# Kernel tuning notes

Measured on AMD Instinct MI355X. Metric: run time of the kernel, lower is better.

The kernel has to match this reference:

```python
import jax, jax.numpy as jnp
import numpy as np

N_CELLS = 50000
HID = 64
DEG = 16
K_NODES = 4  # nodes per cell; cell i owns nodes [4i, 4i+4)
SP = 3


def setup_inputs() -> dict:
    key = jax.random.key(0)
    ks = jax.random.split(key, 12)
    s = 1.0 / np.sqrt(HID)
    inp = {
        'features': jax.random.normal(ks[0], (N_CELLS, HID), jnp.float32),
        'positions': jax.random.normal(ks[1], (K_NODES * N_CELLS, SP), jnp.float32),
        'neighbors': jax.random.randint(ks[2], (N_CELLS, DEG), 0, N_CELLS, jnp.int32),
        # message MLP: Linear(2H+1 -> H), SiLU, Linear(H -> H)
        'W1': jax.random.normal(ks[3], (2 * HID + 1, HID), jnp.float32) * s,
        'b1': jnp.zeros((HID,), jnp.float32),
        'W2': jax.random.normal(ks[4], (HID, HID), jnp.float32) * s,
        'b2': jnp.zeros((HID,), jnp.float32),
        # update MLP: Linear(H + H -> H), SiLU, Linear(H -> H)
        'Wu1': jax.random.normal(ks[5], (2 * HID, HID), jnp.float32) * s,
        'bu1': jnp.zeros((HID,), jnp.float32),
        'Wu2': jax.random.normal(ks[6], (HID, HID), jnp.float32) * s,
        'bu2': jnp.zeros((HID,), jnp.float32),
    }
    return inp


def reference(features, positions, neighbors, W1, b1, W2, b2, Wu1, bu1, Wu2, bu2):
    N, H = features.shape
    # centroid of each cell's owned nodes (cell i -> nodes [K*i, K*i+K))
    cent = positions.reshape(N, K_NODES, SP).mean(axis=1)          # [N, sp]
    fj = features[neighbors]                                       # [N, D, H]
    cj = cent[neighbors]                                           # [N, D, sp]
    # centroid-distance geometric invariant per (cell, neighbor) pair
    geom = jnp.linalg.norm(cent[:, None, :] - cj, axis=-1, keepdims=True)  # [N, D, 1]
    fi = jnp.broadcast_to(features[:, None, :], fj.shape)          # [N, D, H]
    x = jnp.concatenate([fi, fj, geom], axis=-1)                   # [N, D, 2H+1]
    h = jax.nn.silu(x @ W1 + b1) @ W2 + b2                         # [N, D, H]
    msg = h.mean(axis=1)                                           # mean over neighbors
    u = jnp.concatenate([features, msg], axis=-1)                  # [N, 2H]
    upd = jax.nn.silu(u @ Wu1 + bu1) @ Wu2 + bu2
    updated_features = features + upd
    return updated_features, positions
```

## Files before the change

### kernel.cpp

```cpp
#include <hip/hip_runtime.h>


#define DEG 16

typedef __attribute__((ext_vector_type(8))) short short8;
typedef __attribute__((ext_vector_type(4))) float f32x4;
typedef uint2 uint2_a __attribute__((may_alias));
typedef uint4 uint4_a __attribute__((may_alias));

union HbRd { uint4_a u; short8 s; };
union Frag { short8 s; uint4 u; };

__device__ __forceinline__ unsigned f2bf(float f) {
  unsigned u = __float_as_uint(f);
  return (u + 0x7FFFu + ((u >> 16) & 1u)) >> 16;
}
__device__ __forceinline__ float bf2f(unsigned bits16) {
  return __uint_as_float(bits16 << 16);
}
__device__ __forceinline__ float silu(float h) {
  return h / (1.f + __expf(-h));
}
__device__ __forceinline__ float silu_fast(float h) {
  return h * __builtin_amdgcn_rcpf(1.f + __expf(-h));
}

__global__ __launch_bounds__(256) void aux_kernel(
    const float* __restrict__ pos,
    const float* __restrict__ W1, const float* __restrict__ W2,
    const float* __restrict__ Wu1, const float* __restrict__ Wu2,
    float* __restrict__ outpos, float* __restrict__ cent4,
    unsigned short* __restrict__ w1pq, unsigned short* __restrict__ w2t,
    unsigned short* __restrict__ wu1t, unsigned short* __restrict__ wu2b)
{
  int t = blockIdx.x * 256 + threadIdx.x;
  if (t < 150000) {
    ((float4*)outpos)[t] = ((const float4*)pos)[t];
  } else if (t < 174576) {
    const int r = t - 150000;
    if (r < 8192) {
      const int j = r & 7, l = (r >> 3) & 15, q = (r >> 7) & 3;
      const int f = r >> 9, kk = f & 1, mt = f >> 1;
      const int k = kk * 32 + q * 8 + j;
      const int m = mt * 16 + l;
      w1pq[r] = (unsigned short)f2bf(
          (m < 64) ? W1[k * 64 + m] : W1[(k + 64) * 64 + (m - 64)]);
    } else if (r < 12288) {
      const int s = r - 8192;
      const int j = s & 7, l = (s >> 3) & 15, q = (s >> 7) & 3;
      const int f = s >> 9, kk = f & 1, mt = f >> 1;
      const int k = kk * 32 + q * 8 + j;
      w2t[s] = (unsigned short)f2bf(W2[k * 64 + mt * 16 + l]);
    } else if (r < 20480) {
      const int s = r - 12288;
      const int j = s & 7, l = (s >> 3) & 15, q = (s >> 7) & 3;
      const int f = s >> 9, kk = f & 3, mt = f >> 2;
      const int k = kk * 32 + q * 8 + j;
      wu1t[s] = (unsigned short)f2bf(Wu1[k * 64 + mt * 16 + l]);
    } else {
      const int s = r - 20480;
      const int j = s & 7, l = (s >> 3) & 15, q = (s >> 7) & 3;
      const int f = s >> 9, kk = f & 1, nt = f >> 1;
      const int k = kk * 32 + q * 8 + j;
      wu2b[s] = (unsigned short)f2bf(Wu2[k * 64 + nt * 16 + l]);
    }
  } else if (t < 224576) {
    const int i = t - 174576;
    const float4* pp = (const float4*)(pos + 12 * i);
    const float4 a = pp[0], b = pp[1], c = pp[2];
    float4 o;
    o.x = (a.x + a.w + b.z + c.y) * 0.25f;
    o.y = (a.y + b.x + b.w + c.z) * 0.25f;
    o.z = (a.z + b.y + c.x + c.w) * 0.25f;
    o.w = 0.f;
    ((float4*)cent4)[i] = o;
  }
}

__global__ __launch_bounds__(256) void prep_geom_kernel(
    const float* __restrict__ feat,
    const unsigned short* __restrict__ w1pq,
    const float4* __restrict__ cent4,
    const int* __restrict__ nbr,
    unsigned short* __restrict__ featb,
    unsigned short* __restrict__ Pb, unsigned char* __restrict__ Q8,
    float* __restrict__ geomF)
{
  const int b    = blockIdx.x;
  const int lane = threadIdx.x & 63;
  const int wid  = threadIdx.x >> 6;

  if (b >= 782) {
    const int gb  = b - 782;
    const int sub = lane >> 4;
    const int d   = lane & 15;
    const int c   = gb * 16 + wid * 4 + sub;
    const int nj  = nbr[c * DEG + d];
    const float4 ci = cent4[c];
    const float4 cj = cent4[nj];
    const float dx = ci.x - cj.x, dy = ci.y - cj.y, dz = ci.z - cj.z;
    geomF[c * DEG + d] = sqrtf(dx * dx + dy * dy + dz * dz);
    return;
  }

  const int quad = lane >> 4;
  const int l15  = lane & 15;
  const int tile = b * 4 + wid;
  const bool act = (tile < 3125);
  const int  tt  = act ? tile : 3124;
  const int  cr  = tt * 16 + l15;

  short8 xf[2];
  #pragma unroll
  for (int kk = 0; kk < 2; ++kk) {
    const float4 f0 = *(const float4*)(feat + cr * 64 + kk * 32 + quad * 8);
    const float4 f1 = *(const float4*)(feat + cr * 64 + kk * 32 + quad * 8 + 4);
    Frag v;
    v.s[0] = (short)f2bf(f0.x); v.s[1] = (short)f2bf(f0.y);
    v.s[2] = (short)f2bf(f0.z); v.s[3] = (short)f2bf(f0.w);
    v.s[4] = (short)f2bf(f1.x); v.s[5] = (short)f2bf(f1.y);
    v.s[6] = (short)f2bf(f1.z); v.s[7] = (short)f2bf(f1.w);
    xf[kk] = v.s;
    if (act) *(uint4*)(featb + cr * 64 + kk * 32 + quad * 8) = v.u;
  }

  short8 wf[8][2];
  #pragma unroll
  for (int mt = 0; mt < 8; ++mt)
    #pragma unroll
    for (int kk = 0; kk < 2; ++kk)
      wf[mt][kk] = *(const short8*)(w1pq + (((mt * 2 + kk) * 4 + quad) << 7) + l15 * 8);

  f32x4 acc[8] = {};
  #pragma unroll
  for (int kk = 0; kk < 2; ++kk)
    #pragma unroll
    for (int mt = 0; mt < 8; ++mt)
      acc[mt] = __builtin_amdgcn_mfma_f32_16x16x32_bf16(wf[mt][kk], xf[kk], acc[mt], 0, 0, 0);

  if (act) {
    #pragma unroll
    for (int mt = 0; mt < 4; ++mt) {
      uint2 pk;
      pk.x = f2bf(acc[mt][0]) | (f2bf(acc[mt][1]) << 16);
      pk.y = f2bf(acc[mt][2]) | (f2bf(acc[mt][3]) << 16);
      *(uint2*)(Pb + cr * 64 + mt * 16 + quad * 4) = pk;
    }
    #pragma unroll
    for (int mt = 4; mt < 8; ++mt) {
      int w = __builtin_amdgcn_cvt_pk_fp8_f32(acc[mt][0], acc[mt][1], 0, false);
      w = __builtin_amdgcn_cvt_pk_fp8_f32(acc[mt][2], acc[mt][3], w, true);
      *(unsigned int*)(Q8 + cr * 64 + (mt - 4) * 16 + quad * 4) = (unsigned)w;
    }
  }
}

__global__ __launch_bounds__(256) void msg_tail_kernel(
    const unsigned short* __restrict__ featb,
    const unsigned short* __restrict__ Pb,
    const unsigned char* __restrict__ Q8,
    const float* __restrict__ geomF,
    const int* __restrict__ nbr,
    const float* __restrict__ feat,
    const unsigned short* __restrict__ w2t,
    const unsigned short* __restrict__ wu1t,
    const unsigned short* __restrict__ wu2b,
    const float* __restrict__ b1, const float* __restrict__ W1,
    const float* __restrict__ b2, const float* __restrict__ bu1,
    const float* __restrict__ bu2,
    float* __restrict__ outf)
{
  __shared__ uint4 smem[432];
  char* sT  = (char*)smem;
  char* Msg = sT + 2304;
  char* Hb  = sT + 4608;

  const int lane = threadIdx.x & 63;
  const int wid  = threadIdx.x >> 6;
  const int quad = lane >> 4;
  const int l15  = lane & 15;
  const int tile = blockIdx.x;

  const float b1l = b1[lane];
  const float wl  = W1[8192 + lane];

  #pragma unroll
  for (int i = 0; i < 4; ++i) {
    const int c  = tile * 16 + wid * 4 + i;
    const int cs = __builtin_amdgcn_readfirstlane(c);
    const int*   nrow = nbr   + cs * DEG;
    const float* grow = geomF + cs * DEG;

    const float pcb = bf2f(Pb[cs * 64 + lane]) + b1l;

    float acc = 0.f;
    #pragma unroll
    for (int d = 0; d < DEG; ++d) {
      const int   nd = nrow[d];
      const float gd = grow[d];
      const float qv = __builtin_amdgcn_cvt_f32_fp8((int)Q8[nd * 64 + lane], 0);
      acc += silu_fast(pcb + qv + gd * wl);
    }
    ((unsigned short*)(sT + (wid * 4 + i) * 144))[lane] =
        (unsigned short)f2bf(acc * 0.0625f);
  }

  short8 w2f[2], wu1f[4], wu2f[2];
  #pragma unroll
  for (int kk = 0; kk < 2; ++kk)
    w2f[kk]  = *(const short8*)(w2t  + (((wid * 2 + kk) * 4 + quad) << 7) + l15 * 8);
  #pragma unroll
  for (int kk = 0; kk < 4; ++kk)
    wu1f[kk] = *(const short8*)(wu1t + (((wid * 4 + kk) * 4 + quad) << 7) + l15 * 8);
  #pragma unroll
  for (int kk = 0; kk < 2; ++kk)
    wu2f[kk] = *(const short8*)(wu2b + (((wid * 2 + kk) * 4 + quad) << 7) + l15 * 8);

  const f32x4 b2f  = *(const f32x4*)(b2  + wid * 16 + quad * 4);
  const f32x4 bu1f = *(const f32x4*)(bu1 + wid * 16 + quad * 4);
  const float bu2v = bu2[wid * 16 + l15];

  __syncthreads();

  f32x4 accm = {};
  #pragma unroll
  for (int kk = 0; kk < 2; ++kk) {
    HbRd t; t.u = *(const uint4_a*)(sT + l15 * 144 + kk * 64 + quad * 16);
    accm = __builtin_amdgcn_mfma_f32_16x16x32_bf16(w2f[kk], t.s, accm, 0, 0, 0);
  }
  __syncthreads();
  {
    uint2 pk;
    pk.x = f2bf(accm[0] + b2f[0]) | (f2bf(accm[1] + b2f[1]) << 16);
    pk.y = f2bf(accm[2] + b2f[2]) | (f2bf(accm[3] + b2f[3]) << 16);
    *(uint2_a*)(Msg + l15 * 144 + wid * 32 + quad * 8) = pk;
  }
  __syncthreads();

  const int cr = tile * 16 + l15;
  f32x4 accu = {};
  #pragma unroll
  for (int kk = 0; kk < 4; ++kk) {
    short8 bf;
    if (kk < 2) {
      bf = *(const short8*)(featb + cr * 64 + kk * 32 + quad * 8);
    } else {
      HbRd t; t.u = *(const uint4_a*)(Msg + l15 * 144 + (kk - 2) * 64 + quad * 16);
      bf = t.s;
    }
    accu = __builtin_amdgcn_mfma_f32_16x16x32_bf16(wu1f[kk], bf, accu, 0, 0, 0);
  }
  {
    float sv[4];
    #pragma unroll
    for (int rg = 0; rg < 4; ++rg)
      sv[rg] = silu(accu[rg] + bu1f[rg]);
    uint2 pk;
    pk.x = f2bf(sv[0]) | (f2bf(sv[1]) << 16);
    pk.y = f2bf(sv[2]) | (f2bf(sv[3]) << 16);
    *(uint2_a*)(Hb + l15 * 144 + wid * 32 + quad * 8) = pk;
  }
  __syncthreads();

  f32x4 acc2 = {};
  #pragma unroll
  for (int kk = 0; kk < 2; ++kk) {
    HbRd t; t.u = *(const uint4_a*)(Hb + l15 * 144 + kk * 64 + quad * 16);
    acc2 = __builtin_amdgcn_mfma_f32_16x16x32_bf16(t.s, wu2f[kk], acc2, 0, 0, 0);
  }
  #pragma unroll
  for (int rg = 0; rg < 4; ++rg) {
    const int row = tile * 16 + quad * 4 + rg;
    const int col = wid * 16 + l15;
    outf[row * 64 + col] = feat[row * 64 + col] + acc2[rg] + bu2v;
  }
}

extern "C" void kernel_launch(void* const* d_in, const int* in_sizes, int n_in,
                              void* d_out, int out_size, void* d_ws, size_t ws_size,
                              hipStream_t stream)
{
  const float* feat = (const float*)d_in[0];
  const float* pos  = (const float*)d_in[1];
  const int*   nbr  = (const int*)d_in[2];
  const float* W1   = (const float*)d_in[3];
  const float* b1   = (const float*)d_in[4];
  const float* W2   = (const float*)d_in[5];
  const float* b2   = (const float*)d_in[6];
  const float* Wu1  = (const float*)d_in[7];
  const float* bu1  = (const float*)d_in[8];
  const float* Wu2  = (const float*)d_in[9];
  const float* bu2  = (const float*)d_in[10];
  float* out = (float*)d_out;

  unsigned short* featb = (unsigned short*)d_ws;
  unsigned short* Pb    = (unsigned short*)((char*)d_ws + 6400000);
  unsigned char*  Q8    = (unsigned char*)((char*)d_ws + 12800000);
  float*          geomF = (float*)((char*)d_ws + 16000000);
  float*          cent4 = (float*)((char*)d_ws + 25600000);
  unsigned short* w1pq  = (unsigned short*)((char*)d_ws + 26400000);
  unsigned short* w2t   = (unsigned short*)((char*)d_ws + 26416384);
  unsigned short* wu1t  = (unsigned short*)((char*)d_ws + 26424576);
  unsigned short* wu2b  = (unsigned short*)((char*)d_ws + 26440960);

  aux_kernel<<<878, 256, 0, stream>>>(pos, W1, W2, Wu1, Wu2, out + 3200000,
                                      cent4, w1pq, w2t, wu1t, wu2b);
  prep_geom_kernel<<<3907, 256, 0, stream>>>(feat, w1pq, (const float4*)cent4,
                                             nbr, featb, Pb, Q8, geomF);
  msg_tail_kernel<<<3125, 256, 0, stream>>>(featb, Pb, Q8, geomF, nbr, feat,
                                            w2t, wu1t, wu2b,
                                            b1, W1, b2, bu1, bu2, out);
}
```

Measured before the change: 121.8 us.

## Fuse per-cell projection and geometry into message kernel, drop Pb/geomF buffers

The self-feature projection (the Pb half of the W1 product) is now computed inside msg_tail_kernel with MFMA into shared memory instead of being written to and reread from global memory. Centroid distances are computed per lane in the message kernel and broadcast with readlane, which removes the geomF buffer and its extra blocks in the prep kernel. This cuts global traffic and prep work at the cost of extra MFMA, gathers and a barrier in the main kernel. A redundant __syncthreads is also removed because Msg and sT do not overlap.

```diff
diff --git a/kernel.cpp b/kernel.cpp
--- a/kernel.cpp
+++ b/kernel.cpp
@@ -7,6 +7,7 @@
 typedef __attribute__((ext_vector_type(4))) float f32x4;
 typedef uint2 uint2_a __attribute__((may_alias));
 typedef uint4 uint4_a __attribute__((may_alias));
+typedef unsigned short ushort_a __attribute__((may_alias));
 
 union HbRd { uint4_a u; short8 s; };
 union Frag { short8 s; uint4 u; };
@@ -77,35 +78,17 @@
   }
 }
 
-__global__ __launch_bounds__(256) void prep_geom_kernel(
+__global__ __launch_bounds__(256) void prep_kernel(
     const float* __restrict__ feat,
     const unsigned short* __restrict__ w1pq,
-    const float4* __restrict__ cent4,
-    const int* __restrict__ nbr,
     unsigned short* __restrict__ featb,
-    unsigned short* __restrict__ Pb, unsigned char* __restrict__ Q8,
-    float* __restrict__ geomF)
+    unsigned char* __restrict__ Q8)
 {
-  const int b    = blockIdx.x;
   const int lane = threadIdx.x & 63;
   const int wid  = threadIdx.x >> 6;
-
-  if (b >= 782) {
-    const int gb  = b - 782;
-    const int sub = lane >> 4;
-    const int d   = lane & 15;
-    const int c   = gb * 16 + wid * 4 + sub;
-    const int nj  = nbr[c * DEG + d];
-    const float4 ci = cent4[c];
-    const float4 cj = cent4[nj];
-    const float dx = ci.x - cj.x, dy = ci.y - cj.y, dz = ci.z - cj.z;
-    geomF[c * DEG + d] = sqrtf(dx * dx + dy * dy + dz * dz);
-    return;
-  }
-
   const int quad = lane >> 4;
   const int l15  = lane & 15;
-  const int tile = b * 4 + wid;
+  const int tile = blockIdx.x * 4 + wid;
   const bool act = (tile < 3125);
   const int  tt  = act ? tile : 3124;
   const int  cr  = tt * 16 + l15;
@@ -124,44 +107,37 @@
     if (act) *(uint4*)(featb + cr * 64 + kk * 32 + quad * 8) = v.u;
   }
 
-  short8 wf[8][2];
-  #pragma unroll
-  for (int mt = 0; mt < 8; ++mt)
+  short8 wf[4][2];
+  #pragma unroll
+  for (int m = 0; m < 4; ++m)
     #pragma unroll
     for (int kk = 0; kk < 2; ++kk)
-      wf[mt][kk] = *(const short8*)(w1pq + (((mt * 2 + kk) * 4 + quad) << 7) + l15 * 8);
-
-  f32x4 acc[8] = {};
+      wf[m][kk] = *(const short8*)(w1pq + ((((m + 4) * 2 + kk) * 4 + quad) << 7) + l15 * 8);
+
+  f32x4 acc[4] = {};
   #pragma unroll
   for (int kk = 0; kk < 2; ++kk)
     #pragma unroll
-    for (int mt = 0; mt < 8; ++mt)
-      acc[mt] = __builtin_amdgcn_mfma_f32_16x16x32_bf16(wf[mt][kk], xf[kk], acc[mt], 0, 0, 0);
+    for (int m = 0; m < 4; ++m)
+      acc[m] = __builtin_amdgcn_mfma_f32_16x16x32_bf16(wf[m][kk], xf[kk], acc[m], 0, 0, 0);
 
   if (act) {
     #pragma unroll
-    for (int mt = 0; mt < 4; ++mt) {
-      uint2 pk;
-      pk.x = f2bf(acc[mt][0]) | (f2bf(acc[mt][1]) << 16);
-      pk.y = f2bf(acc[mt][2]) | (f2bf(acc[mt][3]) << 16);
-      *(uint2*)(Pb + cr * 64 + mt * 16 + quad * 4) = pk;
-    }
-    #pragma unroll
-    for (int mt = 4; mt < 8; ++mt) {
-      int w = __builtin_amdgcn_cvt_pk_fp8_f32(acc[mt][0], acc[mt][1], 0, false);
-      w = __builtin_amdgcn_cvt_pk_fp8_f32(acc[mt][2], acc[mt][3], w, true);
-      *(unsigned int*)(Q8 + cr * 64 + (mt - 4) * 16 + quad * 4) = (unsigned)w;
+    for (int m = 0; m < 4; ++m) {
+      int w = __builtin_amdgcn_cvt_pk_fp8_f32(acc[m][0], acc[m][1], 0, false);
+      w = __builtin_amdgcn_cvt_pk_fp8_f32(acc[m][2], acc[m][3], w, true);
+      *(unsigned int*)(Q8 + cr * 64 + m * 16 + quad * 4) = (unsigned)w;
     }
   }
 }
 
 __global__ __launch_bounds__(256) void msg_tail_kernel(
     const unsigned short* __restrict__ featb,
-    const unsigned short* __restrict__ Pb,
     const unsigned char* __restrict__ Q8,
-    const float* __restrict__ geomF,
+    const float4* __restrict__ cent4,
     const int* __restrict__ nbr,
     const float* __restrict__ feat,
+    const unsigned short* __restrict__ w1pq,
     const unsigned short* __restrict__ w2t,
     const unsigned short* __restrict__ wu1t,
     const unsigned short* __restrict__ wu2b,
@@ -180,6 +156,26 @@
   const int quad = lane >> 4;
   const int l15  = lane & 15;
   const int tile = blockIdx.x;
+  const int cr   = tile * 16 + l15;
+
+  {
+    short8 wpf[2];
+    #pragma unroll
+    for (int kk = 0; kk < 2; ++kk)
+      wpf[kk] = *(const short8*)(w1pq + (((wid * 2 + kk) * 4 + quad) << 7) + l15 * 8);
+    f32x4 accp = {};
+    #pragma unroll
+    for (int kk = 0; kk < 2; ++kk) {
+      const short8 bf = *(const short8*)(featb + cr * 64 + kk * 32 + quad * 8);
+      accp = __builtin_amdgcn_mfma_f32_16x16x32_bf16(wpf[kk], bf, accp, 0, 0, 0);
+    }
+    uint2 pk;
+    pk.x = f2bf(accp[0]) | (f2bf(accp[1]) << 16);
+    pk.y = f2bf(accp[2]) | (f2bf(accp[3]) << 16);
+    *(uint2_a*)(sT + l15 * 144 + wid * 32 + quad * 8) = pk;
+  }
+
+  __syncthreads();
 
   const float b1l = b1[lane];
   const float wl  = W1[8192 + lane];
@@ -188,20 +184,27 @@
   for (int i = 0; i < 4; ++i) {
     const int c  = tile * 16 + wid * 4 + i;
     const int cs = __builtin_amdgcn_readfirstlane(c);
-    const int*   nrow = nbr   + cs * DEG;
-    const float* grow = geomF + cs * DEG;
-
-    const float pcb = bf2f(Pb[cs * 64 + lane]) + b1l;
+    const int* nrow = nbr + cs * DEG;
+
+    const int njl = nrow[lane & 15];
+    const float4 ci = cent4[cs];
+    const float4 cj = cent4[njl];
+    const float dx = ci.x - cj.x, dy = ci.y - cj.y, dz = ci.z - cj.z;
+    const float g = sqrtf(dx * dx + dy * dy + dz * dz);
+
+    const float pcb =
+        bf2f(((const ushort_a*)(sT + (wid * 4 + i) * 144))[lane]) + b1l;
 
     float acc = 0.f;
     #pragma unroll
     for (int d = 0; d < DEG; ++d) {
       const int   nd = nrow[d];
-      const float gd = grow[d];
+      const float gd = __uint_as_float(
+          __builtin_amdgcn_readlane((int)__float_as_uint(g), d));
       const float qv = __builtin_amdgcn_cvt_f32_fp8((int)Q8[nd * 64 + lane], 0);
       acc += silu_fast(pcb + qv + gd * wl);
     }
-    ((unsigned short*)(sT + (wid * 4 + i) * 144))[lane] =
+    ((ushort_a*)(sT + (wid * 4 + i) * 144))[lane] =
         (unsigned short)f2bf(acc * 0.0625f);
   }
 
@@ -228,7 +231,6 @@
     HbRd t; t.u = *(const uint4_a*)(sT + l15 * 144 + kk * 64 + quad * 16);
     accm = __builtin_amdgcn_mfma_f32_16x16x32_bf16(w2f[kk], t.s, accm, 0, 0, 0);
   }
-  __syncthreads();
   {
     uint2 pk;
     pk.x = f2bf(accm[0] + b2f[0]) | (f2bf(accm[1] + b2f[1]) << 16);
@@ -237,7 +239,6 @@
   }
   __syncthreads();
 
-  const int cr = tile * 16 + l15;
   f32x4 accu = {};
   #pragma unroll
   for (int kk = 0; kk < 4; ++kk) {
@@ -294,9 +295,7 @@
   float* out = (float*)d_out;
 
   unsigned short* featb = (unsigned short*)d_ws;
-  unsigned short* Pb    = (unsigned short*)((char*)d_ws + 6400000);
   unsigned char*  Q8    = (unsigned char*)((char*)d_ws + 12800000);
-  float*          geomF = (float*)((char*)d_ws + 16000000);
   float*          cent4 = (float*)((char*)d_ws + 25600000);
   unsigned short* w1pq  = (unsigned short*)((char*)d_ws + 26400000);
   unsigned short* w2t   = (unsigned short*)((char*)d_ws + 26416384);
@@ -305,9 +304,8 @@
 
   aux_kernel<<<878, 256, 0, stream>>>(pos, W1, W2, Wu1, Wu2, out + 3200000,
                                       cent4, w1pq, w2t, wu1t, wu2b);
-  prep_geom_kernel<<<3907, 256, 0, stream>>>(feat, w1pq, (const float4*)cent4,
-                                             nbr, featb, Pb, Q8, geomF);
-  msg_tail_kernel<<<3125, 256, 0, stream>>>(featb, Pb, Q8, geomF, nbr, feat,
-                                            w2t, wu1t, wu2b,
+  prep_kernel<<<782, 256, 0, stream>>>(feat, w1pq, featb, Q8);
+  msg_tail_kernel<<<3125, 256, 0, stream>>>(featb, Q8, (const float4*)cent4,
+                                            nbr, feat, w1pq, w2t, wu1t, wu2b,
                                             b1, W1, b2, bu1, bu2, out);
 }
```

New measurement: 120.4 us. Within noise of the previous version (-1.1%).
